# Kernel optimization log

Measured on AMD Instinct MI355X. Metric: run time of the kernel, lower is better.

The kernel has to match this reference:

```python
import jax, jax.numpy as jnp
import numpy as np

N = 100000
D = 256
E = 3200000


def setup_inputs() -> dict:
    key = jax.random.key(0)
    ks = jax.random.split(key, 8)
    x = jax.random.normal(ks[0], (N, D), dtype=jnp.float32)
    edge_index = jax.random.randint(ks[1], (2, E), 0, N, dtype=jnp.int64)
    s = 1.0 / np.sqrt(D)
    W_l = jax.random.uniform(ks[2], (D, D), dtype=jnp.float32, minval=-s, maxval=s)
    b_l = jax.random.uniform(ks[3], (D,), dtype=jnp.float32, minval=-s, maxval=s)
    W_r = jax.random.uniform(ks[4], (D, D), dtype=jnp.float32, minval=-s, maxval=s)
    ln_gamma = jnp.ones((D,), dtype=jnp.float32)
    ln_beta = jnp.zeros((D,), dtype=jnp.float32)
    return {"x": x, "edge_index": edge_index, "W_l": W_l, "b_l": b_l,
            "W_r": W_r, "ln_gamma": ln_gamma, "ln_beta": ln_beta}


def reference(x, edge_index, W_l, b_l, W_r, ln_gamma, ln_beta):
    src, dst = edge_index[0], edge_index[1]
    n = x.shape[0]
    # mean aggregation of neighbor (source) features onto destination nodes
    msg_sum = jax.ops.segment_sum(x[src], dst, num_segments=n)        # [N, D]
    deg = jax.ops.segment_sum(jnp.ones((src.shape[0],), x.dtype), dst,
                              num_segments=n)                          # [N]
    agg = msg_sum / jnp.maximum(deg, 1.0)[:, None]
    # SAGEConv: lin_l(agg) + lin_r(x)   (bias in lin_l only)
    f = agg @ W_l.T + b_l + x @ W_r.T
    # exact-erf GELU (torch F.gelu default)
    f = jax.nn.gelu(f, approximate=False)
    # LayerNorm over feature dim
    mu = jnp.mean(f, axis=-1, keepdims=True)
    var = jnp.var(f, axis=-1, keepdims=True)
    f = (f - mu) * jax.lax.rsqrt(var + 1e-5) * ln_gamma + ln_beta
    # dropout in eval mode = identity; residual add
    return f + x
```

## Files before the change

### kernel.cpp

```cpp
#include <hip/hip_runtime.h>

#define D 256
#define KDIM 512
#define BCAP 16384
#define EPB 8192
#define BM 64

typedef __bf16 bf16_t;
typedef bf16_t bf16x8 __attribute__((ext_vector_type(8)));
typedef bf16_t bf16x4 __attribute__((ext_vector_type(4)));
typedef float f32x4_t __attribute__((ext_vector_type(4)));
typedef float f32x2_t __attribute__((ext_vector_type(2)));


__device__ __forceinline__ void scatter_body(int bid, const int* __restrict__ eidx,
                                             int* __restrict__ bcur,
                                             int* __restrict__ staging, int E,
                                             char* smem) {
    int* lhist = (int*)smem;
    int* lcur = lhist + 512;
    int* gbase = lcur + 512;
    const int t = threadIdx.x;
    const int e0 = bid * EPB;
    int e1 = e0 + EPB;
    if (e1 > E) e1 = E;

    lhist[t] = 0;
    lhist[t + 256] = 0;
    lcur[t] = 0;
    lcur[t + 256] = 0;
    __syncthreads();

    for (int e = e0 + t; e < e1; e += 256) {
        int d = eidx[E + e];
        atomicAdd(&lhist[d >> 8], 1);
    }
    __syncthreads();

#pragma unroll
    for (int b = t; b < 512; b += 256) {
        int c = lhist[b];
        gbase[b] = (c > 0) ? atomicAdd(&bcur[b * 16], c) : 0;
    }
    __syncthreads();

    for (int e = e0 + t; e < e1; e += 256) {
        int s = eidx[e];
        int d = eidx[E + e];
        int b = d >> 8;
        int pos = gbase[b] + atomicAdd(&lcur[b], 1);
        staging[(size_t)b * BCAP + pos] = ((d & 255) << 24) | s;
    }
}

__device__ __forceinline__ void bucket_body(int b, const int* __restrict__ bcur,
                                            const int* __restrict__ bbase,
                                            const int* __restrict__ staging,
                                            int* __restrict__ edge_src,
                                            int* __restrict__ row_ptr, int N,
                                            char* smem) {
    int* lhist = (int*)smem;
    int* lscan = lhist + 256;
    int* lcur = lscan + 256;
    int t = threadIdx.x;
    int node_base = b << 8;
    int nn = N - node_base;
    if (nn > 256) nn = 256;
    int cnt = bcur[b * 16];
    int base = bbase[b];
    const int* stg = staging + (size_t)b * BCAP;

    lhist[t] = 0;
    __syncthreads();
    for (int i = t; i < cnt; i += 256)
        atomicAdd(&lhist[((unsigned)stg[i]) >> 24], 1);
    __syncthreads();
    int v = lhist[t];
    lscan[t] = v;
    __syncthreads();
    for (int off = 1; off < 256; off <<= 1) {
        int u = (t >= off) ? lscan[t - off] : 0;
        __syncthreads();
        lscan[t] += u;
        __syncthreads();
    }
    int excl = lscan[t] - v;
    if (t < nn) row_ptr[node_base + t] = base + excl;
    lscan[t] = excl;
    lcur[t] = 0;
    __syncthreads();
    for (int i = t; i < cnt; i += 256) {
        int w = stg[i];
        int ln = ((unsigned)w) >> 24;
        int src = w & 0xFFFFFF;
        int pos = base + lscan[ln] + atomicAdd(&lcur[ln], 1);
        edge_src[pos] = src;
    }
}

__device__ __forceinline__ void gemm_body(int bid, const float* __restrict__ x,
                                          const bf16_t* __restrict__ Wf,
                                          const float* __restrict__ b_l,
                                          unsigned char* __restrict__ Hq,
                                          bf16_t* __restrict__ Hr, int M,
                                          char* smem) {
    bf16_t* A_lds = (bf16_t*)smem;

    const int tid = threadIdx.x;
    const int lane = tid & 63;
    const int wid = tid >> 6;
    const int lr = lane & 15;
    const int lh = lane >> 4;
    const int row0 = bid * BM;

#pragma unroll
    for (int o = 0; o < 8; ++o) {
        int idx = o * 256 + tid;
        int r = idx >> 5;
        int j = idx & 31;
        int gr = row0 + r;
        if (gr > M - 1) gr = M - 1;
        int lb = j ^ (r & 7);
        float4 u0 = *(const float4*)(x + (size_t)gr * D + lb * 8);
        float4 u1 = *(const float4*)(x + (size_t)gr * D + lb * 8 + 4);
        bf16x8 v = {(bf16_t)u0.x, (bf16_t)u0.y, (bf16_t)u0.z, (bf16_t)u0.w,
                    (bf16_t)u1.x, (bf16_t)u1.y, (bf16_t)u1.z, (bf16_t)u1.w};
        *(bf16x8*)&A_lds[idx * 8] = v;
    }
    __syncthreads();

    f32x4_t acc[4][4];

#define KLOOP(P)                                                               \
    _Pragma("unroll") for (int k0 = 0; k0 < 256; k0 += 32) {                   \
        const int kk = k0 >> 5;                                                \
        const int kb = (k0 >> 3) + lh;                                         \
        bf16x8 a[4], b[4];                                                     \
        _Pragma("unroll") for (int mt = 0; mt < 4; mt++) {                     \
            int ra = mt * 16 + lr;                                             \
            a[mt] = *(const bf16x8*)&A_lds[ra * D + ((kb ^ (ra & 7)) << 3)];   \
        }                                                                      \
        _Pragma("unroll") for (int nt = 0; nt < 4; nt++)                       \
            b[nt] = *(const bf16x8*)(wps + ((P) * 65536 + kk * 2048 +          \
                                            nt * 512));                        \
        _Pragma("unroll") for (int mt = 0; mt < 4; mt++)                       \
            _Pragma("unroll") for (int nt = 0; nt < 4; nt++)                   \
                acc[mt][nt] = __builtin_amdgcn_mfma_f32_16x16x32_bf16(         \
                    a[mt], b[nt], acc[mt][nt], 0, 0, 0);                       \
    }

    const bf16_t* wps = Wf + (size_t)wid * 16384 + lane * 8;

#pragma unroll
    for (int i = 0; i < 4; i++)
#pragma unroll
        for (int j = 0; j < 4; j++) acc[i][j] = (f32x4_t){0.f, 0.f, 0.f, 0.f};
    KLOOP(0)
#pragma unroll
    for (int mt = 0; mt < 4; mt++) {
#pragma unroll
        for (int r = 0; r < 4; r++) {
            int m = row0 + mt * 16 + lh * 4 + r;
            if (m < M) {
#pragma unroll
                for (int nt = 0; nt < 4; nt++) {
                    int c = wid * 64 + nt * 16 + lr;
                    float u = acc[mt][nt][r];
                    int w = __builtin_amdgcn_cvt_pk_fp8_f32(u, u, 0, false);
                    Hq[(size_t)m * D + c] = (unsigned char)(w & 0xff);
                }
            }
        }
    }

    float bl[4];
#pragma unroll
    for (int nt = 0; nt < 4; nt++) bl[nt] = b_l[wid * 64 + nt * 16 + lr];
#pragma unroll
    for (int i = 0; i < 4; i++)
#pragma unroll
        for (int j = 0; j < 4; j++) acc[i][j] = (f32x4_t){0.f, 0.f, 0.f, 0.f};
    KLOOP(1)
#undef KLOOP
#pragma unroll
    for (int mt = 0; mt < 4; mt++) {
#pragma unroll
        for (int r = 0; r < 4; r++) {
            int m = row0 + mt * 16 + lh * 4 + r;
            if (m < M) {
#pragma unroll
                for (int nt = 0; nt < 4; nt++) {
                    int c = wid * 64 + nt * 16 + lr;
                    Hr[(size_t)m * D + c] = (bf16_t)(acc[mt][nt][r] + bl[nt]);
                }
            }
        }
    }
}


__global__ __launch_bounds__(256) void k_sg(const int* __restrict__ eidx,
                                            int* __restrict__ bcur,
                                            int* __restrict__ staging, int E,
                                            const float* __restrict__ x,
                                            const bf16_t* __restrict__ Wf,
                                            const float* __restrict__ b_l,
                                            unsigned char* __restrict__ Hq,
                                            bf16_t* __restrict__ Hr, int M,
                                            int nScatter) {
    __shared__ __align__(16) char smem[BM * D * sizeof(bf16_t)];
    int b = blockIdx.x;
    if (b < nScatter)
        scatter_body(b, eidx, bcur, staging, E, smem);
    else
        gemm_body(b - nScatter, x, Wf, b_l, Hq, Hr, M, smem);
}

__global__ __launch_bounds__(256) void k_bg(const int* __restrict__ bcur,
                                            const int* __restrict__ bbase,
                                            const int* __restrict__ staging,
                                            int* __restrict__ edge_src,
                                            int* __restrict__ row_ptr, int N,
                                            const float* __restrict__ x,
                                            const bf16_t* __restrict__ Wf,
                                            const float* __restrict__ b_l,
                                            unsigned char* __restrict__ Hq,
                                            bf16_t* __restrict__ Hr,
                                            int B1, int gemmOff) {
    __shared__ __align__(16) char smem[BM * D * sizeof(bf16_t)];
    int b = blockIdx.x;
    if (b < B1)
        bucket_body(b, bcur, bbase, staging, edge_src, row_ptr, N, smem);
    else
        gemm_body(b - B1 + gemmOff, x, Wf, b_l, Hq, Hr, N, smem);
}

__global__ __launch_bounds__(512) void k_bbase(const int* __restrict__ bcur,
                                               int* __restrict__ bbase,
                                               int* __restrict__ row_ptr,
                                               int B1, int N, int E) {
    __shared__ int sm[512];
    int t = threadIdx.x;
    int v = (t < B1) ? bcur[t * 16] : 0;
    sm[t] = v;
    __syncthreads();
    for (int off = 1; off < 512; off <<= 1) {
        int u = (t >= off) ? sm[t - off] : 0;
        __syncthreads();
        sm[t] += u;
        __syncthreads();
    }
    if (t < B1) bbase[t] = sm[t] - v;
    if (t == 0) row_ptr[N] = E;
}


__global__ __launch_bounds__(256) void k_convw(const float* __restrict__ Wl,
                                               const float* __restrict__ Wr,
                                               bf16_t* __restrict__ Wf) {
    int i = blockIdx.x * 256 + threadIdx.x;
    if (i >= KDIM * D / 4) return;
    int o = i * 4;
    int e = o & 511;
    int c = o >> 9;
    int lane = e >> 3;
    int j0 = e & 7;
    int nt = c & 3;
    int kk = (c >> 2) & 7;
    int s = (c >> 5) & 3;
    int p = c >> 7;
    int row = s * 64 + nt * 16 + (lane & 15);
    int col = kk * 32 + (lane >> 4) * 8 + j0;
    const float* src = (p == 0) ? (Wl + (size_t)row * D + col)
                                : (Wr + (size_t)row * D + col);
    float4 v = *(const float4*)src;
    bf16x4 ov = {(bf16_t)v.x, (bf16_t)v.y, (bf16_t)v.z, (bf16_t)v.w};
    *(bf16x4*)(Wf + o) = ov;
}


__global__ __launch_bounds__(256) void k_final(
        const int* __restrict__ row_ptr, const int* __restrict__ edge_src,
        const unsigned char* __restrict__ Hq, const bf16_t* __restrict__ Hr,
        const float* __restrict__ x, const float* __restrict__ gamma,
        const float* __restrict__ beta, float* __restrict__ out, int N) {
    int wv = threadIdx.x >> 6;
    int lane = threadIdx.x & 63;
    int node = blockIdx.x * 4 + wv;
    if (node >= N) return;
    int g = lane >> 4;
    int c16 = lane & 15;
    int beg = row_ptr[node];
    int end = row_ptr[node + 1];
    const uint4* hb = (const uint4*)Hq;

    f32x2_t acc2[8];
#pragma unroll
    for (int k = 0; k < 8; k++) acc2[k] = (f32x2_t){0.f, 0.f};

#define ACC4(w, i)                                                \
    {                                                             \
        acc2[i] += __builtin_amdgcn_cvt_pk_f32_fp8((w), false);   \
        acc2[(i) + 1] += __builtin_amdgcn_cvt_pk_f32_fp8((w), true); \
    }

    int j = beg;
    for (; j + 8 <= end; j += 8) {
        int s0 = edge_src[j + g];
        int s1 = edge_src[j + 4 + g];
        uint4 v0 = hb[(s0 << 4) + c16];
        uint4 v1 = hb[(s1 << 4) + c16];
        ACC4(v0.x, 0) ACC4(v0.y, 2) ACC4(v0.z, 4) ACC4(v0.w, 6)
        ACC4(v1.x, 0) ACC4(v1.y, 2) ACC4(v1.z, 4) ACC4(v1.w, 6)
    }
    if (j < end) {
        int j0 = j + g, j1 = j + 4 + g;
        bool ok0 = j0 < end, ok1 = j1 < end;
        int s0 = edge_src[ok0 ? j0 : beg];
        int s1 = edge_src[ok1 ? j1 : beg];
        uint4 v0 = hb[(s0 << 4) + c16];
        uint4 v1 = hb[(s1 << 4) + c16];
        if (!ok0) { v0.x = 0; v0.y = 0; v0.z = 0; v0.w = 0; }
        if (!ok1) { v1.x = 0; v1.y = 0; v1.z = 0; v1.w = 0; }
        ACC4(v0.x, 0) ACC4(v0.y, 2) ACC4(v0.z, 4) ACC4(v0.w, 6)
        ACC4(v1.x, 0) ACC4(v1.y, 2) ACC4(v1.z, 4) ACC4(v1.w, 6)
    }
#undef ACC4

    float accf[16];
#pragma unroll
    for (int k = 0; k < 16; k++) accf[k] = acc2[k >> 1][k & 1];
#pragma unroll
    for (int k = 0; k < 16; k++) {
        accf[k] += __shfl_xor(accf[k], 16, 64);
        accf[k] += __shfl_xor(accf[k], 32, 64);
    }
    int dg = end - beg;
    float inv = 1.0f / (float)(dg > 0 ? dg : 1);

    int col0 = c16 * 16 + g * 4;
    bf16x4 hr = *(const bf16x4*)(Hr + (size_t)node * D + col0);
    float v[4];
    float s = 0.f, ss = 0.f;
#pragma unroll
    for (int j2 = 0; j2 < 4; j2++) {
        float t = (g == 0) ? accf[j2]
                : (g == 1) ? accf[4 + j2]
                : (g == 2) ? accf[8 + j2]
                           : accf[12 + j2];
        float u = t * inv + (float)hr[j2];
        float ge = 0.5f * u * (1.0f + erff(u * 0.70710678118654752f));
        v[j2] = ge;
        s += ge;
        ss += ge * ge;
    }
#pragma unroll
    for (int off = 1; off <= 32; off <<= 1) {
        s += __shfl_xor(s, off, 64);
        ss += __shfl_xor(ss, off, 64);
    }
    float mean = s * (1.0f / 256.0f);
    float var = ss * (1.0f / 256.0f) - mean * mean;
    float rstd = rsqrtf(var + 1e-5f);

    float4 ga = *(const float4*)(gamma + col0);
    float4 be = *(const float4*)(beta + col0);
    float4 xr = *(const float4*)(x + (size_t)node * D + col0);
    float4 o;
#pragma unroll
    for (int j2 = 0; j2 < 4; j2++)
        (&o.x)[j2] = (v[j2] - mean) * rstd * (&ga.x)[j2] + (&be.x)[j2] +
                     (&xr.x)[j2];
    *(float4*)(out + (size_t)node * D + col0) = o;
}


extern "C" void kernel_launch(void* const* d_in, const int* in_sizes, int n_in,
                              void* d_out, int out_size, void* d_ws, size_t ws_size,
                              hipStream_t stream) {
    const float* x = (const float*)d_in[0];
    const int* eidx = (const int*)d_in[1];
    const float* W_l = (const float*)d_in[2];
    const float* b_l = (const float*)d_in[3];
    const float* W_r = (const float*)d_in[4];
    const float* gamma = (const float*)d_in[5];
    const float* beta = (const float*)d_in[6];
    float* out = (float*)d_out;

    const int N = in_sizes[0] / D;
    const int E = in_sizes[1] / 2;
    const int B1 = (N + 255) >> 8;
    const int SB = (E + EPB - 1) / EPB;
    const int GB = (N + BM - 1) / BM;
    const int GB1 = (GB + 1) / 2;

    char* basep = (char*)d_ws;
    size_t off = 0;
    auto take = [&](size_t bytes) -> void* {
        void* r = basep + off;
        off += (bytes + 255) & ~(size_t)255;
        return r;
    };
    bf16_t* Hr = (bf16_t*)take((size_t)N * D * sizeof(bf16_t));
    unsigned char* Hq = (unsigned char*)take((size_t)N * D);
    int* staging = (int*)take((size_t)B1 * BCAP * sizeof(int));
    int* edge_src = (int*)take((size_t)E * sizeof(int));
    bf16_t* Wf = (bf16_t*)take((size_t)KDIM * D * sizeof(bf16_t));
    int* row_ptr = (int*)take((size_t)(N + 1) * sizeof(int));
    int* bcur = (int*)take((size_t)B1 * 16 * sizeof(int));
    int* bbase = (int*)take((size_t)B1 * sizeof(int));

    hipMemsetAsync(bcur, 0, (size_t)B1 * 16 * sizeof(int), stream);

    k_convw<<<(KDIM * D / 4 + 255) / 256, 256, 0, stream>>>(W_l, W_r, Wf);

    k_sg<<<SB + GB1, 256, 0, stream>>>(eidx, bcur, staging, E, x, Wf, b_l,
                                       Hq, Hr, N, SB);
    k_bbase<<<1, 512, 0, stream>>>(bcur, bbase, row_ptr, B1, N, E);
    k_bg<<<B1 + (GB - GB1), 256, 0, stream>>>(bcur, bbase, staging, edge_src,
                                              row_ptr, N, x, Wf, b_l, Hq,
                                              Hr, B1, GB1);

    k_final<<<(N + 3) / 4, 256, 0, stream>>>(row_ptr, edge_src, Hq, Hr, x,
                                             gamma, beta, out, N);
}
```

Before: 308.9 us.

## Use 512-thread blocks for scatter, bucket and GEMM phases

Doubles the block size of the fused scatter/GEMM and bucket/GEMM kernels from 256 to 512 threads. In the GEMM part, each of 8 waves now computes a 64x32 output slice instead of 64x64, which halves the per-wave accumulators, and the A-tile load loop is halved. The scatter and bucket loops stride by 512, with guards on the 256-entry scans. The aim is more waves per block to hide latency, at the cost of heavier LDS atomic contention and some idle threads in the scan.

```diff
diff --git a/kernel.cpp b/kernel.cpp
--- a/kernel.cpp
+++ b/kernel.cpp
@@ -26,25 +26,22 @@
     if (e1 > E) e1 = E;
 
     lhist[t] = 0;
-    lhist[t + 256] = 0;
     lcur[t] = 0;
-    lcur[t + 256] = 0;
-    __syncthreads();
-
-    for (int e = e0 + t; e < e1; e += 256) {
+    __syncthreads();
+
+    for (int e = e0 + t; e < e1; e += 512) {
         int d = eidx[E + e];
         atomicAdd(&lhist[d >> 8], 1);
     }
     __syncthreads();
 
-#pragma unroll
-    for (int b = t; b < 512; b += 256) {
-        int c = lhist[b];
-        gbase[b] = (c > 0) ? atomicAdd(&bcur[b * 16], c) : 0;
-    }
-    __syncthreads();
-
-    for (int e = e0 + t; e < e1; e += 256) {
+    {
+        int c = lhist[t];
+        gbase[t] = (c > 0) ? atomicAdd(&bcur[t * 16], c) : 0;
+    }
+    __syncthreads();
+
+    for (int e = e0 + t; e < e1; e += 512) {
         int s = eidx[e];
         int d = eidx[E + e];
         int b = d >> 8;
@@ -70,26 +67,28 @@
     int base = bbase[b];
     const int* stg = staging + (size_t)b * BCAP;
 
-    lhist[t] = 0;
-    __syncthreads();
-    for (int i = t; i < cnt; i += 256)
+    if (t < 256) lhist[t] = 0;
+    __syncthreads();
+    for (int i = t; i < cnt; i += 512)
         atomicAdd(&lhist[((unsigned)stg[i]) >> 24], 1);
     __syncthreads();
-    int v = lhist[t];
-    lscan[t] = v;
+    int v = (t < 256) ? lhist[t] : 0;
+    if (t < 256) lscan[t] = v;
     __syncthreads();
     for (int off = 1; off < 256; off <<= 1) {
-        int u = (t >= off) ? lscan[t - off] : 0;
+        int u = (t >= off && t < 256) ? lscan[t - off] : 0;
         __syncthreads();
-        lscan[t] += u;
+        if (t < 256) lscan[t] += u;
         __syncthreads();
     }
-    int excl = lscan[t] - v;
+    int excl = (t < 256) ? (lscan[t] - v) : 0;
     if (t < nn) row_ptr[node_base + t] = base + excl;
-    lscan[t] = excl;
-    lcur[t] = 0;
-    __syncthreads();
-    for (int i = t; i < cnt; i += 256) {
+    if (t < 256) {
+        lscan[t] = excl;
+        lcur[t] = 0;
+    }
+    __syncthreads();
+    for (int i = t; i < cnt; i += 512) {
         int w = stg[i];
         int ln = ((unsigned)w) >> 24;
         int src = w & 0xFFFFFF;
@@ -112,10 +111,13 @@
     const int lr = lane & 15;
     const int lh = lane >> 4;
     const int row0 = bid * BM;
-
-#pragma unroll
-    for (int o = 0; o < 8; ++o) {
-        int idx = o * 256 + tid;
+    const int cb = wid * 32;
+    const int s4 = wid >> 1;
+    const int nt0 = (wid & 1) * 2;
+
+#pragma unroll
+    for (int o = 0; o < 4; ++o) {
+        int idx = o * 512 + tid;
         int r = idx >> 5;
         int j = idx & 31;
         int gr = row0 + r;
@@ -129,32 +131,32 @@
     }
     __syncthreads();
 
-    f32x4_t acc[4][4];
+    f32x4_t acc[4][2];
+
+    const bf16_t* wps = Wf + (size_t)s4 * 16384 + nt0 * 512 + lane * 8;
 
 #define KLOOP(P)                                                               \
     _Pragma("unroll") for (int k0 = 0; k0 < 256; k0 += 32) {                   \
         const int kk = k0 >> 5;                                                \
         const int kb = (k0 >> 3) + lh;                                         \
-        bf16x8 a[4], b[4];                                                     \
+        bf16x8 a[4], b[2];                                                     \
         _Pragma("unroll") for (int mt = 0; mt < 4; mt++) {                     \
             int ra = mt * 16 + lr;                                             \
             a[mt] = *(const bf16x8*)&A_lds[ra * D + ((kb ^ (ra & 7)) << 3)];   \
         }                                                                      \
-        _Pragma("unroll") for (int nt = 0; nt < 4; nt++)                       \
+        _Pragma("unroll") for (int nt = 0; nt < 2; nt++)                       \
             b[nt] = *(const bf16x8*)(wps + ((P) * 65536 + kk * 2048 +          \
                                             nt * 512));                        \
         _Pragma("unroll") for (int mt = 0; mt < 4; mt++)                       \
-            _Pragma("unroll") for (int nt = 0; nt < 4; nt++)                   \
+            _Pragma("unroll") for (int nt = 0; nt < 2; nt++)                   \
                 acc[mt][nt] = __builtin_amdgcn_mfma_f32_16x16x32_bf16(         \
                     a[mt], b[nt], acc[mt][nt], 0, 0, 0);                       \
     }
 
-    const bf16_t* wps = Wf + (size_t)wid * 16384 + lane * 8;
-
 #pragma unroll
     for (int i = 0; i < 4; i++)
 #pragma unroll
-        for (int j = 0; j < 4; j++) acc[i][j] = (f32x4_t){0.f, 0.f, 0.f, 0.f};
+        for (int j = 0; j < 2; j++) acc[i][j] = (f32x4_t){0.f, 0.f, 0.f, 0.f};
     KLOOP(0)
 #pragma unroll
     for (int mt = 0; mt < 4; mt++) {
@@ -163,8 +165,8 @@
             int m = row0 + mt * 16 + lh * 4 + r;
             if (m < M) {
 #pragma unroll
-                for (int nt = 0; nt < 4; nt++) {
-                    int c = wid * 64 + nt * 16 + lr;
+                for (int nt = 0; nt < 2; nt++) {
+                    int c = cb + nt * 16 + lr;
                     float u = acc[mt][nt][r];
                     int w = __builtin_amdgcn_cvt_pk_fp8_f32(u, u, 0, false);
                     Hq[(size_t)m * D + c] = (unsigned char)(w & 0xff);
@@ -173,13 +175,13 @@
         }
     }
 
-    float bl[4];
-#pragma unroll
-    for (int nt = 0; nt < 4; nt++) bl[nt] = b_l[wid * 64 + nt * 16 + lr];
+    float bl[2];
+#pragma unroll
+    for (int nt = 0; nt < 2; nt++) bl[nt] = b_l[cb + nt * 16 + lr];
 #pragma unroll
     for (int i = 0; i < 4; i++)
 #pragma unroll
-        for (int j = 0; j < 4; j++) acc[i][j] = (f32x4_t){0.f, 0.f, 0.f, 0.f};
+        for (int j = 0; j < 2; j++) acc[i][j] = (f32x4_t){0.f, 0.f, 0.f, 0.f};
     KLOOP(1)
 #undef KLOOP
 #pragma unroll
@@ -189,8 +191,8 @@
             int m = row0 + mt * 16 + lh * 4 + r;
             if (m < M) {
 #pragma unroll
-                for (int nt = 0; nt < 4; nt++) {
-                    int c = wid * 64 + nt * 16 + lr;
+                for (int nt = 0; nt < 2; nt++) {
+                    int c = cb + nt * 16 + lr;
                     Hr[(size_t)m * D + c] = (bf16_t)(acc[mt][nt][r] + bl[nt]);
                 }
             }
@@ -199,7 +201,7 @@
 }
 
 
-__global__ __launch_bounds__(256) void k_sg(const int* __restrict__ eidx,
+__global__ __launch_bounds__(512) void k_sg(const int* __restrict__ eidx,
                                             int* __restrict__ bcur,
                                             int* __restrict__ staging, int E,
                                             const float* __restrict__ x,
@@ -216,7 +218,7 @@
         gemm_body(b - nScatter, x, Wf, b_l, Hq, Hr, M, smem);
 }
 
-__global__ __launch_bounds__(256) void k_bg(const int* __restrict__ bcur,
+__global__ __launch_bounds__(512) void k_bg(const int* __restrict__ bcur,
                                             const int* __restrict__ bbase,
                                             const int* __restrict__ staging,
                                             int* __restrict__ edge_src,
@@ -414,10 +416,10 @@
 
     k_convw<<<(KDIM * D / 4 + 255) / 256, 256, 0, stream>>>(W_l, W_r, Wf);
 
-    k_sg<<<SB + GB1, 256, 0, stream>>>(eidx, bcur, staging, E, x, Wf, b_l,
+    k_sg<<<SB + GB1, 512, 0, stream>>>(eidx, bcur, staging, E, x, Wf, b_l,
                                        Hq, Hr, N, SB);
     k_bbase<<<1, 512, 0, stream>>>(bcur, bbase, row_ptr, B1, N, E);
-    k_bg<<<B1 + (GB - GB1), 256, 0, stream>>>(bcur, bbase, staging, edge_src,
+    k_bg<<<B1 + (GB - GB1), 512, 0, stream>>>(bcur, bbase, staging, edge_src,
                                               row_ptr, N, x, Wf, b_l, Hq,
                                               Hr, B1, GB1);
 
```

Result: faster. 281.1 us (-9.0%).
